# Kernel optimization log

Hardware: AMD Instinct MI355X
Metric: run time of the kernel (lower is better)

Reference implementation:

```python
import jax, jax.numpy as jnp
import numpy as np

S, B, L, D, H, NOP = 4, 8, 512, 128, 128, 64  # segments, batch, seg_len, input_dim, hidden, n_operators
W = S * L  # 2048 total words
FT = 0.1   # forget-gate floor


def _norm_mat(m):
    # divide each row by its count of nonzero entries (torch normalize_matrix)
    cnt = (m != 0).sum(-1, keepdims=True).astype(m.dtype)
    return m / (cnt + 1e-30)


def _l2(x):
    return x / (jnp.linalg.norm(x, axis=-1, keepdims=True) + 1e-30)


def setup_inputs() -> dict:
    key = jax.random.key(0)
    ks = jax.random.split(key, 16)
    word_outputs = jax.random.normal(ks[0], (S, B, L, D), jnp.float32)
    node_hidden = jax.random.normal(ks[1], (B, D), jnp.float32)
    op_embedding = jax.random.normal(ks[2], (B, NOP, D), jnp.float32)
    word_operator = (jax.random.uniform(ks[3], (B, W, NOP)) < 0.05).astype(jnp.float32)
    word_word = (jax.random.uniform(ks[4], (B, W, W)) < 0.02).astype(jnp.float32)
    depend_relation = (jax.random.uniform(ks[5], (S, B, L, L)) < 0.05).astype(jnp.float32)
    word_exist_matrix = (jax.random.uniform(ks[6], (B, W, W)) < 0.9).astype(jnp.float32)
    word_exist_sequence = (jax.random.uniform(ks[7], (B, W)) < 0.9).astype(jnp.float32)
    goal_word = (jax.random.uniform(ks[8], (B, W)) < 0.2).astype(jnp.float32)

    def lin(k, fi, fo):
        k1, k2 = jax.random.split(k)
        s = 1.0 / np.sqrt(fi).astype(np.float32)
        return (jax.random.uniform(k1, (fi, fo), jnp.float32, -s, s),
                jax.random.uniform(k2, (fo,), jnp.float32, -s, s))

    o_w_W, o_w_b = lin(ks[9], D, H)
    wk_W, wk_b = lin(ks[10], D, H)
    ws_W, ws_b = lin(ks[11], D, H)
    up_W, up_b = lin(ks[12], 3 * H, D)
    wg_W, wg_b = lin(ks[13], D, D)
    fg_W, fg_b = lin(ks[14], 2 * D, D)
    return dict(word_outputs=word_outputs, node_hidden=node_hidden, op_embedding=op_embedding,
                word_operator=word_operator, word_word=word_word, depend_relation=depend_relation,
                word_exist_matrix=word_exist_matrix, word_exist_sequence=word_exist_sequence,
                goal_word=goal_word, o_w_W=o_w_W, o_w_b=o_w_b, wk_W=wk_W, wk_b=wk_b,
                ws_W=ws_W, ws_b=ws_b, up_W=up_W, up_b=up_b, wg_W=wg_W, wg_b=wg_b,
                fg_W=fg_W, fg_b=fg_b)


def reference(word_outputs, node_hidden, op_embedding, word_operator, word_word,
              depend_relation, word_exist_matrix, word_exist_sequence, goal_word,
              o_w_W, o_w_b, wk_W, wk_b, ws_W, ws_b, up_W, up_b, wg_W, wg_b, fg_W, fg_b):
    # cat(word_outputs, dim=1) -> [B, W, D]
    all_word = word_outputs.transpose(1, 0, 2, 3).reshape(B, W, D)
    # operator aggregation: [B,W,NOP] @ o_w(op_embedding) -> [B,W,H], L2-normalized
    word_o = _l2(jnp.einsum('bwo,boh->bwh', word_operator, op_embedding @ o_w_W + o_w_b))
    # knowledge aggregation over masked word-word adjacency
    adj_k = _norm_mat(word_word * word_exist_matrix)
    word_w_k = _l2(jnp.einsum('bvw,bwh->bvh', adj_k, all_word @ wk_W + wk_b))
    # per-segment dependency aggregation, then concat along word dim
    seg = jnp.einsum('sbij,sbjh->sbih', _norm_mat(depend_relation), word_outputs @ ws_W + ws_b)
    word_w_s = _l2(seg.transpose(1, 0, 2, 3).reshape(B, W, H))
    neighbor = jnp.concatenate([word_o, word_w_k, word_w_s], axis=-1)  # [B, W, 3H]
    word_updated = jax.nn.relu(neighbor @ up_W + up_b)  # [B, W, D]
    # goal pooling: bmm([B,1,W],[B,W,D]) -> [B,D]
    gw = _norm_mat(goal_word * word_exist_sequence)
    goal_w = jnp.einsum('bw,bwd->bd', gw, word_updated)
    goal_updated = jax.nn.relu(goal_w @ wg_W + wg_b)
    forget = jax.nn.sigmoid(jnp.concatenate([goal_w, node_hidden], axis=-1) @ fg_W + fg_b)
    return jnp.maximum(forget, FT) * node_hidden + (1.0 - forget) * goal_updated
```

## Files before the change

### kernel.cpp

```cpp
#include <hip/hip_runtime.h>
#include <math.h>

#define Sn 4
#define Bn 8
#define Ln 512
#define Dn 128
#define Hn 128
#define NOPn 64
#define Wn 2048


__device__ __forceinline__ float bf2f(unsigned short u) {
    return __uint_as_float(((unsigned int)u) << 16);
}
__device__ __forceinline__ float bflo(unsigned int u) {
    return __uint_as_float(u << 16);
}
__device__ __forceinline__ float bfhi(unsigned int u) {
    return __uint_as_float(u & 0xFFFF0000u);
}
__device__ __forceinline__ unsigned short f2bf(float f) {
    unsigned int u = __float_as_uint(f);
    return (unsigned short)((u + 0x7FFFu + ((u >> 16) & 1u)) >> 16);
}

__global__ __launch_bounds__(256) void prep_k(const float* __restrict__ A,
                                              const float* __restrict__ W1,
                                              const float* __restrict__ W2,
                                              const float* __restrict__ b1,
                                              const float* __restrict__ b2,
                                              unsigned short* __restrict__ C1,
                                              unsigned short* __restrict__ C2,
                                              const float* __restrict__ ope,
                                              const float* __restrict__ owW,
                                              const float* __restrict__ owb,
                                              unsigned short* __restrict__ oph,
                                              const float* __restrict__ goal,
                                              const float* __restrict__ wes,
                                              int* __restrict__ widx,
                                              int* __restrict__ wcnt,
                                              float* __restrict__ gwacc,
                                              const float* __restrict__ upW,
                                              unsigned short* __restrict__ upWbf) {
    __shared__ __align__(16) float lA[32][68];
    __shared__ __align__(16) float lW1[32][132];
    __shared__ __align__(16) float lW2[32][132];
    __shared__ int cnt;
    const int bid = blockIdx.x, tid = threadIdx.x;

    if (bid < 256) {
        const int m0 = bid * 64;
        float acc1[4][8] = {}, acc2[4][8] = {};
        const int r0 = (tid & 15) * 4;
        const int h0 = (tid >> 4) * 8;
        for (int k0 = 0; k0 < 128; k0 += 32) {
            __syncthreads();
            {
                const int r = tid >> 2, kk = (tid & 3) * 8;
                const float* src = A + (size_t)(m0 + r) * 128 + (k0 + kk);
                float4 v0 = reinterpret_cast<const float4*>(src)[0];
                float4 v1 = reinterpret_cast<const float4*>(src)[1];
                lA[kk + 0][r] = v0.x; lA[kk + 1][r] = v0.y;
                lA[kk + 2][r] = v0.z; lA[kk + 3][r] = v0.w;
                lA[kk + 4][r] = v1.x; lA[kk + 5][r] = v1.y;
                lA[kk + 6][r] = v1.z; lA[kk + 7][r] = v1.w;
            }
            {
                const int kk = tid >> 3, hh = (tid & 7) * 16;
                const float* s1 = W1 + (size_t)(k0 + kk) * 128 + hh;
                const float* s2 = W2 + (size_t)(k0 + kk) * 128 + hh;
#pragma unroll
                for (int q = 0; q < 4; ++q) {
                    float4 v1 = reinterpret_cast<const float4*>(s1)[q];
                    float4 v2 = reinterpret_cast<const float4*>(s2)[q];
                    lW1[kk][hh + 4 * q + 0] = v1.x; lW1[kk][hh + 4 * q + 1] = v1.y;
                    lW1[kk][hh + 4 * q + 2] = v1.z; lW1[kk][hh + 4 * q + 3] = v1.w;
                    lW2[kk][hh + 4 * q + 0] = v2.x; lW2[kk][hh + 4 * q + 1] = v2.y;
                    lW2[kk][hh + 4 * q + 2] = v2.z; lW2[kk][hh + 4 * q + 3] = v2.w;
                }
            }
            __syncthreads();
#pragma unroll
            for (int k = 0; k < 32; ++k) {
                float4 a   = *reinterpret_cast<const float4*>(&lA[k][r0]);
                float4 w10 = *reinterpret_cast<const float4*>(&lW1[k][h0]);
                float4 w11 = *reinterpret_cast<const float4*>(&lW1[k][h0 + 4]);
                float4 w20 = *reinterpret_cast<const float4*>(&lW2[k][h0]);
                float4 w21 = *reinterpret_cast<const float4*>(&lW2[k][h0 + 4]);
                float av[4] = {a.x, a.y, a.z, a.w};
                float wv1[8] = {w10.x, w10.y, w10.z, w10.w, w11.x, w11.y, w11.z, w11.w};
                float wv2[8] = {w20.x, w20.y, w20.z, w20.w, w21.x, w21.y, w21.z, w21.w};
#pragma unroll
                for (int i = 0; i < 4; ++i)
#pragma unroll
                    for (int j = 0; j < 8; ++j) {
                        acc1[i][j] = fmaf(av[i], wv1[j], acc1[i][j]);
                        acc2[i][j] = fmaf(av[i], wv2[j], acc2[i][j]);
                    }
            }
        }
#pragma unroll
        for (int i = 0; i < 4; ++i) {
            alignas(16) unsigned short u1[8], u2[8];
#pragma unroll
            for (int j = 0; j < 8; ++j) {
                u1[j] = f2bf(acc1[i][j] + b1[h0 + j]);
                u2[j] = f2bf(acc2[i][j] + b2[h0 + j]);
            }
            const size_t off = (size_t)(m0 + r0 + i) * 128 + h0;
            *reinterpret_cast<uint4*>(C1 + off) = *reinterpret_cast<const uint4*>(u1);
            *reinterpret_cast<uint4*>(C2 + off) = *reinterpret_cast<const uint4*>(u2);
        }
    } else if (bid < 264) {
        const int m0 = (bid - 256) * 64;
        float acc[4][8] = {};
        const int r0 = (tid & 15) * 4;
        const int h0 = (tid >> 4) * 8;
        for (int k0 = 0; k0 < 128; k0 += 32) {
            __syncthreads();
            {
                const int r = tid >> 2, kk = (tid & 3) * 8;
                const float* src = ope + (size_t)(m0 + r) * 128 + (k0 + kk);
                float4 v0 = reinterpret_cast<const float4*>(src)[0];
                float4 v1 = reinterpret_cast<const float4*>(src)[1];
                lA[kk + 0][r] = v0.x; lA[kk + 1][r] = v0.y;
                lA[kk + 2][r] = v0.z; lA[kk + 3][r] = v0.w;
                lA[kk + 4][r] = v1.x; lA[kk + 5][r] = v1.y;
                lA[kk + 6][r] = v1.z; lA[kk + 7][r] = v1.w;
            }
            {
                const int kk = tid >> 3, hh = (tid & 7) * 16;
                const float* src = owW + (size_t)(k0 + kk) * 128 + hh;
#pragma unroll
                for (int q = 0; q < 4; ++q) {
                    float4 v = reinterpret_cast<const float4*>(src)[q];
                    lW1[kk][hh + 4 * q + 0] = v.x; lW1[kk][hh + 4 * q + 1] = v.y;
                    lW1[kk][hh + 4 * q + 2] = v.z; lW1[kk][hh + 4 * q + 3] = v.w;
                }
            }
            __syncthreads();
#pragma unroll
            for (int k = 0; k < 32; ++k) {
                float4 a  = *reinterpret_cast<const float4*>(&lA[k][r0]);
                float4 w0 = *reinterpret_cast<const float4*>(&lW1[k][h0]);
                float4 w1 = *reinterpret_cast<const float4*>(&lW1[k][h0 + 4]);
                float av[4] = {a.x, a.y, a.z, a.w};
                float wv[8] = {w0.x, w0.y, w0.z, w0.w, w1.x, w1.y, w1.z, w1.w};
#pragma unroll
                for (int i = 0; i < 4; ++i)
#pragma unroll
                    for (int j = 0; j < 8; ++j) acc[i][j] = fmaf(av[i], wv[j], acc[i][j]);
            }
        }
#pragma unroll
        for (int i = 0; i < 4; ++i) {
            alignas(16) unsigned short us[8];
#pragma unroll
            for (int j = 0; j < 8; ++j) us[j] = f2bf(acc[i][j] + owb[h0 + j]);
            *reinterpret_cast<uint4*>(oph + (size_t)(m0 + r0 + i) * 128 + h0) =
                *reinterpret_cast<const uint4*>(us);
        }
    } else if (bid < 272) {
        const int b = bid - 264;
        if (tid == 0) cnt = 0;
        __syncthreads();
#pragma unroll
        for (int j = 0; j < 8; ++j) {
            const int w = tid * 8 + j;
            if (goal[b * Wn + w] != 0.f && wes[b * Wn + w] != 0.f) {
                const int p = atomicAdd(&cnt, 1);
                if (p < 512) widx[b * 512 + p] = w;
            }
        }
        __syncthreads();
        if (tid == 0) wcnt[b] = cnt < 512 ? cnt : 512;
    } else if (bid == 272) {
        for (int idx = tid; idx < 1024; idx += 256) gwacc[idx] = 0.f;
    } else {
        const int base = (bid - 273) * 24576;
        for (int e = base + tid * 4; e < base + 24576; e += 1024) {
            float4 v = *reinterpret_cast<const float4*>(upW + e);
            alignas(8) unsigned short u[4] = {f2bf(v.x), f2bf(v.y), f2bf(v.z), f2bf(v.w)};
            *reinterpret_cast<uint2*>(upWbf + e) = *reinterpret_cast<const uint2*>(u);
        }
    }
}

__global__ __launch_bounds__(256) void mega_agg5(const int* __restrict__ widx,
                                                 const int* __restrict__ wcnt,
                                                 const float* __restrict__ ww,
                                                 const float* __restrict__ wem,
                                                 const float* __restrict__ dep,
                                                 const float* __restrict__ wop,
                                                 const unsigned short* __restrict__ oph,
                                                 const unsigned short* __restrict__ wkh,
                                                 const unsigned short* __restrict__ wsh,
                                                 const unsigned short* __restrict__ upWbf,
                                                 const float* __restrict__ upb,
                                                 float* __restrict__ gwacc) {
    const int slot = blockIdx.x;
    const int b = slot >> 9, i = slot & 511;
    if (i >= wcnt[b]) return;
    const int w_dst = widx[slot];
    const int t = threadIdx.x;
    const int lane = t & 63, wv = t >> 6;

    __shared__ int kidx[512];
    __shared__ int sidx[256];
    __shared__ int kn, sn;
    __shared__ float part1[4][128];
    __shared__ float part2[4][128];
    __shared__ float nbL[384];
    __shared__ float gp16[16][128];
    if (t == 0) { kn = 0; sn = 0; }
    __syncthreads();

    const float* wwr = ww  + ((size_t)(b * Wn + w_dst)) * Wn;
    const float* wmr = wem + ((size_t)(b * Wn + w_dst)) * Wn;
#pragma unroll
    for (int q = 0; q < 2; ++q) {
        const int e0 = q * 1024 + t * 4;
        float4 v = *reinterpret_cast<const float4*>(wwr + e0);
        float4 m = *reinterpret_cast<const float4*>(wmr + e0);
        float vv[4] = {v.x, v.y, v.z, v.w};
        float mm[4] = {m.x, m.y, m.z, m.w};
#pragma unroll
        for (int j = 0; j < 4; ++j)
            if (vv[j] != 0.f && mm[j] != 0.f) {
                int p = atomicAdd(&kn, 1);
                if (p < 512) kidx[p] = e0 + j;
            }
    }
    const int sD = w_dst >> 9, lD = w_dst & 511;
    if (t < 128) {
        const float* dr = dep + ((size_t)((sD * Bn + b) * Ln + lD)) * Ln + t * 4;
        float4 v = *reinterpret_cast<const float4*>(dr);
        float vv[4] = {v.x, v.y, v.z, v.w};
#pragma unroll
        for (int j = 0; j < 4; ++j)
            if (vv[j] != 0.f) {
                int p = atomicAdd(&sn, 1);
                if (p < 256) sidx[p] = t * 4 + j;
            }
    }
    float m_op = 0.f;
    if (wv == 3) m_op = wop[((size_t)(b * Wn + w_dst)) * NOPn + lane];
    __syncthreads();

    const int nk = kn < 512 ? kn : 512;
    const int ns = sn < 256 ? sn : 256;

    {
        const int hl = lane >> 5, c = lane & 31;
        float a0 = 0.f, a1 = 0.f, a2 = 0.f, a3 = 0.f;
        for (int p = wv * 2 + hl; p < nk; p += 8) {
            const int w = kidx[p];
            const int s = w >> 9, l = w & 511;
            ushort4 x = *reinterpret_cast<const ushort4*>(
                wkh + ((size_t)((s * Bn + b) * Ln + l)) * Hn + c * 4);
            a0 += bf2f(x.x); a1 += bf2f(x.y); a2 += bf2f(x.z); a3 += bf2f(x.w);
        }
        a0 += __shfl_xor(a0, 32); a1 += __shfl_xor(a1, 32);
        a2 += __shfl_xor(a2, 32); a3 += __shfl_xor(a3, 32);
        if (hl == 0) {
            part1[wv][c * 4 + 0] = a0; part1[wv][c * 4 + 1] = a1;
            part1[wv][c * 4 + 2] = a2; part1[wv][c * 4 + 3] = a3;
        }
    }
    {
        const int hl = lane >> 5, c = lane & 31;
        const unsigned short* base = wsh + (size_t)((sD * Bn + b) * Ln) * Hn + c * 4;
        float a0 = 0.f, a1 = 0.f, a2 = 0.f, a3 = 0.f;
        for (int p = wv * 2 + hl; p < ns; p += 8) {
            ushort4 x = *reinterpret_cast<const ushort4*>(base + (size_t)sidx[p] * Hn);
            a0 += bf2f(x.x); a1 += bf2f(x.y); a2 += bf2f(x.z); a3 += bf2f(x.w);
        }
        a0 += __shfl_xor(a0, 32); a1 += __shfl_xor(a1, 32);
        a2 += __shfl_xor(a2, 32); a3 += __shfl_xor(a3, 32);
        if (hl == 0) {
            part2[wv][c * 4 + 0] = a0; part2[wv][c * 4 + 1] = a1;
            part2[wv][c * 4 + 2] = a2; part2[wv][c * 4 + 3] = a3;
        }
    }
    if (wv == 3) {
        unsigned long long bal = __ballot(m_op != 0.f);
        float a0 = 0.f, a1 = 0.f;
        const unsigned short* base = oph + (size_t)b * NOPn * Hn + 2 * lane;
        while (bal) {
            const int o = __ffsll(bal) - 1;
            bal &= bal - 1;
            ushort2 v = *reinterpret_cast<const ushort2*>(base + o * Hn);
            a0 += bf2f(v.x);
            a1 += bf2f(v.y);
        }
        float ss = a0 * a0 + a1 * a1;
#pragma unroll
        for (int off = 1; off < 64; off <<= 1) ss += __shfl_xor(ss, off);
        const float sc = 1.f / (sqrtf(ss) + 1e-30f);
        nbL[2 * lane]     = a0 * sc;
        nbL[2 * lane + 1] = a1 * sc;
    }
    __syncthreads();

    if (wv == 0) {
        float s0 = 0.f, s1 = 0.f;
#pragma unroll
        for (int q = 0; q < 4; ++q) {
            s0 += part1[q][2 * lane];
            s1 += part1[q][2 * lane + 1];
        }
        float ss = s0 * s0 + s1 * s1;
#pragma unroll
        for (int off = 1; off < 64; off <<= 1) ss += __shfl_xor(ss, off);
        const float sc = 1.f / (sqrtf(ss) + 1e-30f);
        nbL[128 + 2 * lane]     = s0 * sc;
        nbL[128 + 2 * lane + 1] = s1 * sc;
    } else if (wv == 1) {
        float s0 = 0.f, s1 = 0.f;
#pragma unroll
        for (int q = 0; q < 4; ++q) {
            s0 += part2[q][2 * lane];
            s1 += part2[q][2 * lane + 1];
        }
        float ss = s0 * s0 + s1 * s1;
#pragma unroll
        for (int off = 1; off < 64; off <<= 1) ss += __shfl_xor(ss, off);
        const float sc = 1.f / (sqrtf(ss) + 1e-30f);
        nbL[256 + 2 * lane]     = s0 * sc;
        nbL[256 + 2 * lane + 1] = s1 * sc;
    }
    __syncthreads();

    {
        const int i8 = (t & 15) * 8, j = t >> 4;
        float a[8] = {};
#pragma unroll
        for (int r = 0; r < 24; ++r) {
            const int k = r * 16 + j;
            const uint4 w = *reinterpret_cast<const uint4*>(upWbf + (size_t)k * 128 + i8);
            const float x = nbL[k];
            a[0] = fmaf(x, bflo(w.x), a[0]); a[1] = fmaf(x, bfhi(w.x), a[1]);
            a[2] = fmaf(x, bflo(w.y), a[2]); a[3] = fmaf(x, bfhi(w.y), a[3]);
            a[4] = fmaf(x, bflo(w.z), a[4]); a[5] = fmaf(x, bfhi(w.z), a[5]);
            a[6] = fmaf(x, bflo(w.w), a[6]); a[7] = fmaf(x, bfhi(w.w), a[7]);
        }
#pragma unroll
        for (int q = 0; q < 8; ++q) gp16[j][i8 + q] = a[q];
    }
    __syncthreads();
    if (t < 128) {
        float g = upb[t];
#pragma unroll
        for (int j = 0; j < 16; ++j) g += gp16[j][t];
        g = fmaxf(g, 0.f);
        atomicAdd(&gwacc[b * 128 + t], g);
    }
}

__global__ __launch_bounds__(128) void final4_k(const int* __restrict__ wcnt,
                                                const float* __restrict__ gwacc,
                                                const float* __restrict__ nh,
                                                const float* __restrict__ wgW,
                                                const float* __restrict__ wgb,
                                                const float* __restrict__ fgW,
                                                const float* __restrict__ fgb,
                                                float* __restrict__ out) {
    const int b = blockIdx.x, t = threadIdx.x;
    __shared__ float gw[Dn], nhs[Dn];
    const float inv = 1.f / ((float)wcnt[b] + 1e-30f);
    gw[t]  = gwacc[b * Dn + t] * inv;
    nhs[t] = nh[b * Dn + t];
    __syncthreads();
    float gu = wgb[t];
    for (int d = 0; d < Dn; ++d) gu = fmaf(gw[d], wgW[d * Dn + t], gu);
    gu = fmaxf(gu, 0.f);
    float fg = fgb[t];
    for (int d = 0; d < Dn; ++d) fg = fmaf(gw[d], fgW[d * Dn + t], fg);
    for (int d = 0; d < Dn; ++d) fg = fmaf(nhs[d], fgW[(Dn + d) * Dn + t], fg);
    const float forget = 1.f / (1.f + expf(-fg));
    out[b * Dn + t] = fmaxf(forget, 0.1f) * nhs[t] + (1.f - forget) * gu;
}

extern "C" void kernel_launch(void* const* d_in, const int* in_sizes, int n_in,
                              void* d_out, int out_size, void* d_ws, size_t ws_size,
                              hipStream_t stream) {
    (void)in_sizes; (void)n_in; (void)out_size; (void)ws_size;
    const float* word_outputs        = (const float*)d_in[0];
    const float* node_hidden         = (const float*)d_in[1];
    const float* op_embedding        = (const float*)d_in[2];
    const float* word_operator       = (const float*)d_in[3];
    const float* word_word           = (const float*)d_in[4];
    const float* depend_relation     = (const float*)d_in[5];
    const float* word_exist_matrix   = (const float*)d_in[6];
    const float* word_exist_sequence = (const float*)d_in[7];
    const float* goal_word           = (const float*)d_in[8];
    const float* o_w_W = (const float*)d_in[9];
    const float* o_w_b = (const float*)d_in[10];
    const float* wk_W  = (const float*)d_in[11];
    const float* wk_b  = (const float*)d_in[12];
    const float* ws_W  = (const float*)d_in[13];
    const float* ws_b  = (const float*)d_in[14];
    const float* up_W  = (const float*)d_in[15];
    const float* up_b  = (const float*)d_in[16];
    const float* wg_W  = (const float*)d_in[17];
    const float* wg_b  = (const float*)d_in[18];
    const float* fg_W  = (const float*)d_in[19];
    const float* fg_b  = (const float*)d_in[20];
    float* out = (float*)d_out;

    char* ws = (char*)d_ws;
    unsigned short* oph   = (unsigned short*)(ws + 0);
    unsigned short* wkh   = (unsigned short*)(ws + (1u << 20));
    unsigned short* wsh   = (unsigned short*)(ws + (5u << 20));
    int* widx             = (int*)(ws + (9u << 20));
    int* wcnt             = (int*)(ws + (9u << 20) + 32768);
    float* gwacc          = (float*)(ws + (9u << 20) + 65536);
    unsigned short* upWbf = (unsigned short*)(ws + (9u << 20) + 131072);

    prep_k<<<275, 256, 0, stream>>>(word_outputs, wk_W, ws_W, wk_b, ws_b, wkh, wsh,
                                    op_embedding, o_w_W, o_w_b, oph,
                                    goal_word, word_exist_sequence, widx, wcnt, gwacc,
                                    up_W, upWbf);
    mega_agg5<<<4096, 256, 0, stream>>>(widx, wcnt, word_word, word_exist_matrix,
                                        depend_relation, word_operator, oph, wkh, wsh,
                                        upWbf, up_b, gwacc);
    final4_k<<<8, 128, 0, stream>>>(wcnt, gwacc, node_hidden,
                                    wg_W, wg_b, fg_W, fg_b, out);
}
```

Before: 345.0 us.

## Process two goal words per block in aggregation kernel to share up_W loads

Each block of the aggregation kernel now handles two destination words instead of one, so grid size halves. Row scans, gathers, and the bf16 up-projection are interleaved for both words, and each up_W load is reused for two FMA streams. This targets per-block overhead and duplicate weight traffic. In exchange it uses more registers and shared memory, which may lower occupancy, and the gather loops run to the larger of the two counts.

```diff
diff --git a/kernel.cpp b/kernel.cpp
--- a/kernel.cpp
+++ b/kernel.cpp
@@ -186,7 +186,7 @@
     }
 }
 
-__global__ __launch_bounds__(256) void mega_agg5(const int* __restrict__ widx,
+__global__ __launch_bounds__(256) void mega_agg6(const int* __restrict__ widx,
                                                  const int* __restrict__ wcnt,
                                                  const float* __restrict__ ww,
                                                  const float* __restrict__ wem,
@@ -198,91 +198,152 @@
                                                  const unsigned short* __restrict__ upWbf,
                                                  const float* __restrict__ upb,
                                                  float* __restrict__ gwacc) {
-    const int slot = blockIdx.x;
-    const int b = slot >> 9, i = slot & 511;
-    if (i >= wcnt[b]) return;
-    const int w_dst = widx[slot];
+    const int bid = blockIdx.x;
+    const int b = bid >> 8, pr = bid & 255;
+    const int wc = wcnt[b];
+    const int i0 = pr * 2;
+    if (i0 >= wc) return;
+    const bool has1 = (i0 + 1) < wc;
+    const int w0 = widx[b * 512 + i0];
+    const int w1 = has1 ? widx[b * 512 + i0 + 1] : w0;
     const int t = threadIdx.x;
     const int lane = t & 63, wv = t >> 6;
 
-    __shared__ int kidx[512];
-    __shared__ int sidx[256];
-    __shared__ int kn, sn;
-    __shared__ float part1[4][128];
-    __shared__ float part2[4][128];
-    __shared__ float nbL[384];
+    __shared__ int kidx[2][512];
+    __shared__ int sidx[2][256];
+    __shared__ int kn[2], sn[2];
+    __shared__ float part1[2][4][128];
+    __shared__ float part2[2][4][128];
+    __shared__ float nbL[2][384];
     __shared__ float gp16[16][128];
-    if (t == 0) { kn = 0; sn = 0; }
+    if (t == 0) { kn[0] = 0; kn[1] = 0; sn[0] = 0; sn[1] = 0; }
     __syncthreads();
 
-    const float* wwr = ww  + ((size_t)(b * Wn + w_dst)) * Wn;
-    const float* wmr = wem + ((size_t)(b * Wn + w_dst)) * Wn;
+    const float* wwr0 = ww  + ((size_t)(b * Wn + w0)) * Wn;
+    const float* wmr0 = wem + ((size_t)(b * Wn + w0)) * Wn;
+    const float* wwr1 = ww  + ((size_t)(b * Wn + w1)) * Wn;
+    const float* wmr1 = wem + ((size_t)(b * Wn + w1)) * Wn;
 #pragma unroll
     for (int q = 0; q < 2; ++q) {
         const int e0 = q * 1024 + t * 4;
-        float4 v = *reinterpret_cast<const float4*>(wwr + e0);
-        float4 m = *reinterpret_cast<const float4*>(wmr + e0);
-        float vv[4] = {v.x, v.y, v.z, v.w};
-        float mm[4] = {m.x, m.y, m.z, m.w};
-#pragma unroll
-        for (int j = 0; j < 4; ++j)
-            if (vv[j] != 0.f && mm[j] != 0.f) {
-                int p = atomicAdd(&kn, 1);
-                if (p < 512) kidx[p] = e0 + j;
-            }
-    }
-    const int sD = w_dst >> 9, lD = w_dst & 511;
+        float4 v0 = *reinterpret_cast<const float4*>(wwr0 + e0);
+        float4 m0 = *reinterpret_cast<const float4*>(wmr0 + e0);
+        float4 v1 = *reinterpret_cast<const float4*>(wwr1 + e0);
+        float4 m1 = *reinterpret_cast<const float4*>(wmr1 + e0);
+        float vv0[4] = {v0.x, v0.y, v0.z, v0.w};
+        float mm0[4] = {m0.x, m0.y, m0.z, m0.w};
+        float vv1[4] = {v1.x, v1.y, v1.z, v1.w};
+        float mm1[4] = {m1.x, m1.y, m1.z, m1.w};
+#pragma unroll
+        for (int j = 0; j < 4; ++j) {
+            if (vv0[j] != 0.f && mm0[j] != 0.f) {
+                int p = atomicAdd(&kn[0], 1);
+                if (p < 512) kidx[0][p] = e0 + j;
+            }
+            if (vv1[j] != 0.f && mm1[j] != 0.f) {
+                int p = atomicAdd(&kn[1], 1);
+                if (p < 512) kidx[1][p] = e0 + j;
+            }
+        }
+    }
+    const int sD0 = w0 >> 9, lD0 = w0 & 511;
+    const int sD1 = w1 >> 9, lD1 = w1 & 511;
     if (t < 128) {
-        const float* dr = dep + ((size_t)((sD * Bn + b) * Ln + lD)) * Ln + t * 4;
-        float4 v = *reinterpret_cast<const float4*>(dr);
-        float vv[4] = {v.x, v.y, v.z, v.w};
-#pragma unroll
-        for (int j = 0; j < 4; ++j)
-            if (vv[j] != 0.f) {
-                int p = atomicAdd(&sn, 1);
-                if (p < 256) sidx[p] = t * 4 + j;
-            }
+        const float* dr0 = dep + ((size_t)((sD0 * Bn + b) * Ln + lD0)) * Ln + t * 4;
+        const float* dr1 = dep + ((size_t)((sD1 * Bn + b) * Ln + lD1)) * Ln + t * 4;
+        float4 v0 = *reinterpret_cast<const float4*>(dr0);
+        float4 v1 = *reinterpret_cast<const float4*>(dr1);
+        float vv0[4] = {v0.x, v0.y, v0.z, v0.w};
+        float vv1[4] = {v1.x, v1.y, v1.z, v1.w};
+#pragma unroll
+        for (int j = 0; j < 4; ++j) {
+            if (vv0[j] != 0.f) {
+                int p = atomicAdd(&sn[0], 1);
+                if (p < 256) sidx[0][p] = t * 4 + j;
+            }
+            if (vv1[j] != 0.f) {
+                int p = atomicAdd(&sn[1], 1);
+                if (p < 256) sidx[1][p] = t * 4 + j;
+            }
+        }
     }
     float m_op = 0.f;
-    if (wv == 3) m_op = wop[((size_t)(b * Wn + w_dst)) * NOPn + lane];
+    if (wv == 3)      m_op = wop[((size_t)(b * Wn + w0)) * NOPn + lane];
+    else if (wv == 2) m_op = wop[((size_t)(b * Wn + w1)) * NOPn + lane];
     __syncthreads();
 
-    const int nk = kn < 512 ? kn : 512;
-    const int ns = sn < 256 ? sn : 256;
+    const int nk0 = kn[0] < 512 ? kn[0] : 512;
+    const int nk1 = kn[1] < 512 ? kn[1] : 512;
+    const int ns0 = sn[0] < 256 ? sn[0] : 256;
+    const int ns1 = sn[1] < 256 ? sn[1] : 256;
+    const int hl = lane >> 5, c = lane & 31;
 
     {
-        const int hl = lane >> 5, c = lane & 31;
-        float a0 = 0.f, a1 = 0.f, a2 = 0.f, a3 = 0.f;
-        for (int p = wv * 2 + hl; p < nk; p += 8) {
-            const int w = kidx[p];
-            const int s = w >> 9, l = w & 511;
-            ushort4 x = *reinterpret_cast<const ushort4*>(
-                wkh + ((size_t)((s * Bn + b) * Ln + l)) * Hn + c * 4);
-            a0 += bf2f(x.x); a1 += bf2f(x.y); a2 += bf2f(x.z); a3 += bf2f(x.w);
-        }
-        a0 += __shfl_xor(a0, 32); a1 += __shfl_xor(a1, 32);
-        a2 += __shfl_xor(a2, 32); a3 += __shfl_xor(a3, 32);
+        float aA[4] = {}, aB[4] = {};
+        const int pm = nk0 > nk1 ? nk0 : nk1;
+        for (int p = wv * 2 + hl; p < pm; p += 8) {
+            if (p < nk0) {
+                const int w = kidx[0][p];
+                const int s = w >> 9, l = w & 511;
+                ushort4 x = *reinterpret_cast<const ushort4*>(
+                    wkh + ((size_t)((s * Bn + b) * Ln + l)) * Hn + c * 4);
+                aA[0] += bf2f(x.x); aA[1] += bf2f(x.y);
+                aA[2] += bf2f(x.z); aA[3] += bf2f(x.w);
+            }
+            if (p < nk1) {
+                const int w = kidx[1][p];
+                const int s = w >> 9, l = w & 511;
+                ushort4 x = *reinterpret_cast<const ushort4*>(
+                    wkh + ((size_t)((s * Bn + b) * Ln + l)) * Hn + c * 4);
+                aB[0] += bf2f(x.x); aB[1] += bf2f(x.y);
+                aB[2] += bf2f(x.z); aB[3] += bf2f(x.w);
+            }
+        }
+#pragma unroll
+        for (int q = 0; q < 4; ++q) {
+            aA[q] += __shfl_xor(aA[q], 32);
+            aB[q] += __shfl_xor(aB[q], 32);
+        }
         if (hl == 0) {
-            part1[wv][c * 4 + 0] = a0; part1[wv][c * 4 + 1] = a1;
-            part1[wv][c * 4 + 2] = a2; part1[wv][c * 4 + 3] = a3;
+#pragma unroll
+            for (int q = 0; q < 4; ++q) {
+                part1[0][wv][c * 4 + q] = aA[q];
+                part1[1][wv][c * 4 + q] = aB[q];
+            }
         }
     }
     {
-        const int hl = lane >> 5, c = lane & 31;
-        const unsigned short* base = wsh + (size_t)((sD * Bn + b) * Ln) * Hn + c * 4;
-        float a0 = 0.f, a1 = 0.f, a2 = 0.f, a3 = 0.f;
-        for (int p = wv * 2 + hl; p < ns; p += 8) {
-            ushort4 x = *reinterpret_cast<const ushort4*>(base + (size_t)sidx[p] * Hn);
-            a0 += bf2f(x.x); a1 += bf2f(x.y); a2 += bf2f(x.z); a3 += bf2f(x.w);
-        }
-        a0 += __shfl_xor(a0, 32); a1 += __shfl_xor(a1, 32);
-        a2 += __shfl_xor(a2, 32); a3 += __shfl_xor(a3, 32);
+        const unsigned short* base0 = wsh + (size_t)((sD0 * Bn + b) * Ln) * Hn + c * 4;
+        const unsigned short* base1 = wsh + (size_t)((sD1 * Bn + b) * Ln) * Hn + c * 4;
+        float aA[4] = {}, aB[4] = {};
+        const int pm = ns0 > ns1 ? ns0 : ns1;
+        for (int p = wv * 2 + hl; p < pm; p += 8) {
+            if (p < ns0) {
+                ushort4 x = *reinterpret_cast<const ushort4*>(base0 + (size_t)sidx[0][p] * Hn);
+                aA[0] += bf2f(x.x); aA[1] += bf2f(x.y);
+                aA[2] += bf2f(x.z); aA[3] += bf2f(x.w);
+            }
+            if (p < ns1) {
+                ushort4 x = *reinterpret_cast<const ushort4*>(base1 + (size_t)sidx[1][p] * Hn);
+                aB[0] += bf2f(x.x); aB[1] += bf2f(x.y);
+                aB[2] += bf2f(x.z); aB[3] += bf2f(x.w);
+            }
+        }
+#pragma unroll
+        for (int q = 0; q < 4; ++q) {
+            aA[q] += __shfl_xor(aA[q], 32);
+            aB[q] += __shfl_xor(aB[q], 32);
+        }
         if (hl == 0) {
-            part2[wv][c * 4 + 0] = a0; part2[wv][c * 4 + 1] = a1;
-            part2[wv][c * 4 + 2] = a2; part2[wv][c * 4 + 3] = a3;
-        }
-    }
-    if (wv == 3) {
+#pragma unroll
+            for (int q = 0; q < 4; ++q) {
+                part2[0][wv][c * 4 + q] = aA[q];
+                part2[1][wv][c * 4 + q] = aB[q];
+            }
+        }
+    }
+    if (wv >= 2) {
+        const int u = 3 - wv;
         unsigned long long bal = __ballot(m_op != 0.f);
         float a0 = 0.f, a1 = 0.f;
         const unsigned short* base = oph + (size_t)b * NOPn * Hn + 2 * lane;
@@ -297,63 +358,82 @@
 #pragma unroll
         for (int off = 1; off < 64; off <<= 1) ss += __shfl_xor(ss, off);
         const float sc = 1.f / (sqrtf(ss) + 1e-30f);
-        nbL[2 * lane]     = a0 * sc;
-        nbL[2 * lane + 1] = a1 * sc;
+        nbL[u][2 * lane]     = a0 * sc;
+        nbL[u][2 * lane + 1] = a1 * sc;
     }
     __syncthreads();
 
-    if (wv == 0) {
-        float s0 = 0.f, s1 = 0.f;
-#pragma unroll
-        for (int q = 0; q < 4; ++q) {
-            s0 += part1[q][2 * lane];
-            s1 += part1[q][2 * lane + 1];
-        }
-        float ss = s0 * s0 + s1 * s1;
-#pragma unroll
-        for (int off = 1; off < 64; off <<= 1) ss += __shfl_xor(ss, off);
-        const float sc = 1.f / (sqrtf(ss) + 1e-30f);
-        nbL[128 + 2 * lane]     = s0 * sc;
-        nbL[128 + 2 * lane + 1] = s1 * sc;
-    } else if (wv == 1) {
-        float s0 = 0.f, s1 = 0.f;
-#pragma unroll
-        for (int q = 0; q < 4; ++q) {
-            s0 += part2[q][2 * lane];
-            s1 += part2[q][2 * lane + 1];
-        }
-        float ss = s0 * s0 + s1 * s1;
-#pragma unroll
-        for (int off = 1; off < 64; off <<= 1) ss += __shfl_xor(ss, off);
-        const float sc = 1.f / (sqrtf(ss) + 1e-30f);
-        nbL[256 + 2 * lane]     = s0 * sc;
-        nbL[256 + 2 * lane + 1] = s1 * sc;
+    {
+        const int u = wv & 1;
+        if (wv < 2) {
+            float s0 = 0.f, s1 = 0.f;
+#pragma unroll
+            for (int q = 0; q < 4; ++q) {
+                s0 += part1[u][q][2 * lane];
+                s1 += part1[u][q][2 * lane + 1];
+            }
+            float ss = s0 * s0 + s1 * s1;
+#pragma unroll
+            for (int off = 1; off < 64; off <<= 1) ss += __shfl_xor(ss, off);
+            const float sc = 1.f / (sqrtf(ss) + 1e-30f);
+            nbL[u][128 + 2 * lane]     = s0 * sc;
+            nbL[u][128 + 2 * lane + 1] = s1 * sc;
+        } else {
+            float s0 = 0.f, s1 = 0.f;
+#pragma unroll
+            for (int q = 0; q < 4; ++q) {
+                s0 += part2[u][q][2 * lane];
+                s1 += part2[u][q][2 * lane + 1];
+            }
+            float ss = s0 * s0 + s1 * s1;
+#pragma unroll
+            for (int off = 1; off < 64; off <<= 1) ss += __shfl_xor(ss, off);
+            const float sc = 1.f / (sqrtf(ss) + 1e-30f);
+            nbL[u][256 + 2 * lane]     = s0 * sc;
+            nbL[u][256 + 2 * lane + 1] = s1 * sc;
+        }
     }
     __syncthreads();
 
-    {
-        const int i8 = (t & 15) * 8, j = t >> 4;
-        float a[8] = {};
-#pragma unroll
-        for (int r = 0; r < 24; ++r) {
-            const int k = r * 16 + j;
-            const uint4 w = *reinterpret_cast<const uint4*>(upWbf + (size_t)k * 128 + i8);
-            const float x = nbL[k];
-            a[0] = fmaf(x, bflo(w.x), a[0]); a[1] = fmaf(x, bfhi(w.x), a[1]);
-            a[2] = fmaf(x, bflo(w.y), a[2]); a[3] = fmaf(x, bfhi(w.y), a[3]);
-            a[4] = fmaf(x, bflo(w.z), a[4]); a[5] = fmaf(x, bfhi(w.z), a[5]);
-            a[6] = fmaf(x, bflo(w.w), a[6]); a[7] = fmaf(x, bfhi(w.w), a[7]);
-        }
-#pragma unroll
-        for (int q = 0; q < 8; ++q) gp16[j][i8 + q] = a[q];
-    }
+    const int i8 = (t & 15) * 8, j = t >> 4;
+    float aA[8] = {}, aB[8] = {};
+#pragma unroll
+    for (int r = 0; r < 24; ++r) {
+        const int k = r * 16 + j;
+        const uint4 w = *reinterpret_cast<const uint4*>(upWbf + (size_t)k * 128 + i8);
+        const float x0 = nbL[0][k], x1 = nbL[1][k];
+        float wl;
+        wl = bflo(w.x); aA[0] = fmaf(x0, wl, aA[0]); aB[0] = fmaf(x1, wl, aB[0]);
+        wl = bfhi(w.x); aA[1] = fmaf(x0, wl, aA[1]); aB[1] = fmaf(x1, wl, aB[1]);
+        wl = bflo(w.y); aA[2] = fmaf(x0, wl, aA[2]); aB[2] = fmaf(x1, wl, aB[2]);
+        wl = bfhi(w.y); aA[3] = fmaf(x0, wl, aA[3]); aB[3] = fmaf(x1, wl, aB[3]);
+        wl = bflo(w.z); aA[4] = fmaf(x0, wl, aA[4]); aB[4] = fmaf(x1, wl, aB[4]);
+        wl = bfhi(w.z); aA[5] = fmaf(x0, wl, aA[5]); aB[5] = fmaf(x1, wl, aB[5]);
+        wl = bflo(w.w); aA[6] = fmaf(x0, wl, aA[6]); aB[6] = fmaf(x1, wl, aB[6]);
+        wl = bfhi(w.w); aA[7] = fmaf(x0, wl, aA[7]); aB[7] = fmaf(x1, wl, aB[7]);
+    }
+#pragma unroll
+    for (int q = 0; q < 8; ++q) gp16[j][i8 + q] = aA[q];
     __syncthreads();
     if (t < 128) {
         float g = upb[t];
 #pragma unroll
-        for (int j = 0; j < 16; ++j) g += gp16[j][t];
+        for (int jj = 0; jj < 16; ++jj) g += gp16[jj][t];
         g = fmaxf(g, 0.f);
         atomicAdd(&gwacc[b * 128 + t], g);
+    }
+    if (has1) {
+        __syncthreads();
+#pragma unroll
+        for (int q = 0; q < 8; ++q) gp16[j][i8 + q] = aB[q];
+        __syncthreads();
+        if (t < 128) {
+            float g = upb[t];
+#pragma unroll
+            for (int jj = 0; jj < 16; ++jj) g += gp16[jj][t];
+            g = fmaxf(g, 0.f);
+            atomicAdd(&gwacc[b * 128 + t], g);
+        }
     }
 }
 
@@ -421,7 +501,7 @@
                                     op_embedding, o_w_W, o_w_b, oph,
                                     goal_word, word_exist_sequence, widx, wcnt, gwacc,
                                     up_W, upWbf);
-    mega_agg5<<<4096, 256, 0, stream>>>(widx, wcnt, word_word, word_exist_matrix,
+    mega_agg6<<<2048, 256, 0, stream>>>(widx, wcnt, word_word, word_exist_matrix,
                                         depend_relation, word_operator, oph, wkh, wsh,
                                         upWbf, up_b, gwacc);
     final4_k<<<8, 128, 0, stream>>>(wcnt, gwacc, node_hidden,
```

Measured after the change: 361.7 us. 4.8% more time.
